# Optimization experiments

Measured on AMD Instinct MI355X. Metric: run time of the kernel, lower is better.

Reference implementation:

```python
import jax, jax.numpy as jnp
import numpy as np


def setup_inputs() -> dict:
    key = jax.random.key(0)
    ks = jax.random.split(key, 7)
    B, T, IN_F = 16384, 64, 48
    F = 32          # feature_size = len(INTERACTIVE_LIST)
    H = 128         # embedding_hidden_size
    TF, TH = T * F, T * H
    scale1 = 1.0 / np.sqrt(TF)
    scale2 = 1.0 / np.sqrt(TH)
    return {
        "x": jax.random.normal(ks[0], (B, T, IN_F), dtype=jnp.float32),
        "W1": jax.random.normal(ks[1], (TF, TH), dtype=jnp.float32) * scale1,
        "b1": jax.random.normal(ks[2], (TH,), dtype=jnp.float32) * scale1,
        "W2": jax.random.normal(ks[3], (TH, TF), dtype=jnp.float32) * scale2,
        "b2": jax.random.normal(ks[4], (TF,), dtype=jnp.float32) * scale2,
        "weight": jax.random.normal(ks[5], (T, F), dtype=jnp.float32),
        "bias": jax.random.normal(ks[6], (F,), dtype=jnp.float32) * (1.0 / np.sqrt(T)),
        "sample_index": jnp.arange(F, dtype=jnp.int32),
    }


def reference(x, W1, b1, W2, b2, weight, bias, sample_index):
    # x: [B, T, IN_F]; gather interactive feature columns -> [B, T, F]
    B = x.shape[0]
    T, F = weight.shape
    xs = jnp.take(x, sample_index, axis=2)            # [B, T, F]
    # pass_linear=True path: MLP on flattened time*feature vector
    h = jax.nn.relu(xs.reshape(B, T * F) @ W1 + b1)   # [B, T*H]; dropout = identity (eval)
    out = (h @ W2 + b2).reshape(B, T, F)              # [B, T, F]
    # vectorized form of the per-sample loop: sum over time of elementwise mul
    emb = jnp.einsum("btf,tf->bf", out, weight) + bias  # [B, F]
    return emb
```

## Files before the change

kernel.cpp:

```cpp
#include <hip/hip_runtime.h>
#include <hip/hip_bf16.h>

#define BATCH 16384
#define TT    64
#define INF   48
#define FF    32
#define TFD   2048
#define THD   8192

typedef __attribute__((ext_vector_type(8))) short bf16x8;
typedef __attribute__((ext_vector_type(4))) short bf16x4;
typedef __attribute__((ext_vector_type(4))) short short4v;
typedef __attribute__((ext_vector_type(4))) float f32x4;

__device__ inline void gload_lds16(const void* g, void* l) {
  __builtin_amdgcn_global_load_lds((const __attribute__((address_space(1))) void*)g,
                                   (__attribute__((address_space(3))) void*)l, 16, 0, 0);
}

__device__ inline f32x4 mfma16x16x16_bf16(bf16x4 a, bf16x4 b, f32x4 c) {
#if __has_builtin(__builtin_amdgcn_mfma_f32_16x16x16bf16_1k)
  return __builtin_amdgcn_mfma_f32_16x16x16bf16_1k(a, b, c, 0, 0, 0);
#else
  asm("v_mfma_f32_16x16x16_bf16 %0, %1, %2, %0" : "+v"(c) : "v"(a), "v"(b));
  return c;
#endif
}

__device__ inline short f32_to_bf16_bits(float x) {
  __hip_bfloat16 h = __float2bfloat16(x);
  return *reinterpret_cast<short*>(&h);
}


__global__ void gather_cast_frag(const float* __restrict__ x, const int* __restrict__ sidx,
                                 __hip_bfloat16* __restrict__ xsf) {
  __shared__ int sx[FF];
  if (threadIdx.x < FF) sx[threadIdx.x] = sidx[threadIdx.x];
  __syncthreads();
  const int b64 = blockIdx.x >> 2;
  const int tq  = blockIdx.x & 3;
  for (int it = 0; it < 16; ++it) {
    const int slot = (tq * 16 + it) * 256 + threadIdx.x;
    const int t  = slot >> 8;
    const int bi = (slot >> 6) & 3;
    const int l  = slot & 63;
    const int lo = l & 15, hi = l >> 4;
    const int row = b64 * 64 + bi * 16 + lo;
    const float* rp = x + ((size_t)row * TT + t) * INF;
    bf16x8 v;
    #pragma unroll
    for (int j = 0; j < 8; ++j) v[j] = f32_to_bf16_bits(rp[sx[hi * 8 + j]]);
    *(bf16x8*)(xsf + ((size_t)b64 * 16384 + slot) * 8) = v;
  }
}

__global__ void transpose_w1(const float* __restrict__ W1, __hip_bfloat16* __restrict__ W1t) {
  __shared__ float tile[64][65];
  const int k0 = blockIdx.x * 64;
  const int n0 = blockIdx.y * 64;
  const int tx = threadIdx.x & 63, ty = threadIdx.x >> 6;
  for (int r = ty; r < 64; r += 4)
    tile[r][tx] = W1[(size_t)(k0 + r) * THD + n0 + tx];
  __syncthreads();
  const int rn = threadIdx.x >> 4;
  const int kq = (threadIdx.x & 15) * 4;
  for (int rr = rn; rr < 64; rr += 16) {
    short4v v;
    #pragma unroll
    for (int i = 0; i < 4; ++i) v[i] = f32_to_bf16_bits(tile[kq + i][rr]);
    *(short4v*)(W1t + (size_t)(n0 + rr) * TFD + k0 + kq) = v;
  }
}

__global__ void make_w2eff(const float* __restrict__ W2, const float* __restrict__ b2,
                           const float* __restrict__ weight, const float* __restrict__ bias,
                           __hip_bfloat16* __restrict__ w2t, float* __restrict__ beff) {
  const int n = blockIdx.x * 8 + (threadIdx.x >> 5);
  const int f = threadIdx.x & 31;
  const float* wr = W2 + (size_t)n * TFD;
  float s = 0.f;
  #pragma unroll 8
  for (int t = 0; t < TT; ++t) s += wr[t * FF + f] * weight[t * FF + f];
  w2t[(size_t)f * THD + n] = __float2bfloat16(s);
  if (blockIdx.x == 0 && threadIdx.x < FF) {
    float sb = bias[f];
    for (int t = 0; t < TT; ++t) sb += b2[t * FF + f] * weight[t * FF + f];
    beff[f] = sb;
  }
}


__device__ inline void stage_w(char* buf, const __hip_bfloat16* __restrict__ w1t,
                               int n0, int k0, int wid, int l) {
  const int sub = l >> 3;
  const int c   = (l & 7) ^ sub;
  const int h   = c >> 2, kc = c & 3;
  const int r0  = wid * 8 + sub;
  const __hip_bfloat16* gw0 = w1t + (size_t)(n0 + 2 * r0 + h) * TFD + k0 + kc * 8;
  const __hip_bfloat16* gw1 = w1t + (size_t)(n0 + 128 + 2 * r0 + h) * TFD + k0 + kc * 8;
  char* lx = buf + wid * 1024;
  gload_lds16(gw0, lx);
  gload_lds16(gw1, lx + 8192);
}

__device__ __forceinline__ void k_iter(char* lds, int t, int n0,
    const char* __restrict__ xbase, const __hip_bfloat16* __restrict__ w1t,
    f32x4 (&acc)[8][4], bf16x8 (&xfu)[4],
    int wbase, int wid, int l, bool do_bar) {
  if (t <= 60) stage_w(lds + ((t + 3) & 7) * 16384, w1t, n0, (t + 3) * 32, wid, l);
  __builtin_amdgcn_sched_barrier(0);
  const char* buf = lds + (t & 7) * 16384;
  bf16x8 w0  = *(const bf16x8*)(buf + wbase);
  bf16x8 w1f = *(const bf16x8*)(buf + wbase + 1024);
  #pragma unroll
  for (int g = 0; g < 4; ++g) {
    bf16x8 nw0, nw1;
    if (g < 3) {
      nw0 = *(const bf16x8*)(buf + wbase + (2 * g + 2) * 1024);
      nw1 = *(const bf16x8*)(buf + wbase + (2 * g + 3) * 1024);
    }
    __builtin_amdgcn_s_setprio(1);
    #pragma unroll
    for (int bi = 0; bi < 4; ++bi)
      acc[2 * g][bi] = __builtin_amdgcn_mfma_f32_16x16x32_bf16(w0, xfu[bi], acc[2 * g][bi], 0, 0, 0);
    #pragma unroll
    for (int bi = 0; bi < 4; ++bi)
      acc[2 * g + 1][bi] = __builtin_amdgcn_mfma_f32_16x16x32_bf16(w1f, xfu[bi], acc[2 * g + 1][bi], 0, 0, 0);
    __builtin_amdgcn_s_setprio(0);
    if (g < 3) { w0 = nw0; w1f = nw1; }
  }
  if (t <= 61) {
    #pragma unroll
    for (int bi = 0; bi < 4; ++bi)
      xfu[bi] = *(const bf16x8*)(xbase + ((t + 2) * 4 + bi) * 1024);
  }
  __builtin_amdgcn_sched_barrier(0);
  if (t <= 60)      asm volatile("s_waitcnt vmcnt(6)" ::: "memory");
  else if (t == 61) asm volatile("s_waitcnt vmcnt(4)" ::: "memory");
  else              asm volatile("s_waitcnt vmcnt(0)" ::: "memory");
  __builtin_amdgcn_sched_barrier(0);
  if (do_bar) {
    __builtin_amdgcn_s_barrier();
    __builtin_amdgcn_sched_barrier(0);
  }
}

__global__ __launch_bounds__(512, 2) void gemm_fused(
    const __hip_bfloat16* __restrict__ xsf,
    const __hip_bfloat16* __restrict__ w1t,
    const float* __restrict__ b1,
    const __hip_bfloat16* __restrict__ w2t,
    float* __restrict__ partial)
{
  __shared__ __align__(16) char lds[131072];
  const int tid = threadIdx.x;
  const int wid = tid >> 6, l = tid & 63;
  const int mq = wid >> 2, bq = wid & 3;
  const int lo = l & 15, hi = l >> 4;
  const int rl = lo >> 1;
  const int cofs = (((((lo & 1) << 2) | hi) ^ rl) << 4);
  const int strip = blockIdx.x & 7;
  const int bt = blockIdx.x >> 3;
  const int b0 = bt * 256;

  const int wbase = ((mq << 6) + rl) * 128 + cofs;
  const char* xbase = (const char*)xsf + ((size_t)(bt * 4 + bq) * 16384 + l) * 16;

  f32x4 acc2[2][4];
  #pragma unroll
  for (int fi = 0; fi < 2; ++fi)
    #pragma unroll
    for (int bi = 0; bi < 4; ++bi) { f32x4 z = {0.f,0.f,0.f,0.f}; acc2[fi][bi] = z; }

  for (int s = 0; s < 4; ++s) {
    const int n0 = strip * 1024 + s * 256;

    f32x4 acc[8][4];
    #pragma unroll
    for (int mi = 0; mi < 8; ++mi)
      #pragma unroll
      for (int bi = 0; bi < 4; ++bi) { f32x4 z = {0.f,0.f,0.f,0.f}; acc[mi][bi] = z; }

    bf16x8 xfA[4], xfB[4];
    stage_w(lds, w1t, n0, 0, wid, l);
    __builtin_amdgcn_sched_barrier(0);
    #pragma unroll
    for (int bi = 0; bi < 4; ++bi) xfA[bi] = *(const bf16x8*)(xbase + (0 * 4 + bi) * 1024);
    __builtin_amdgcn_sched_barrier(0);
    stage_w(lds + 16384, w1t, n0, 32, wid, l);
    __builtin_amdgcn_sched_barrier(0);
    #pragma unroll
    for (int bi = 0; bi < 4; ++bi) xfB[bi] = *(const bf16x8*)(xbase + (1 * 4 + bi) * 1024);
    __builtin_amdgcn_sched_barrier(0);
    stage_w(lds + 32768, w1t, n0, 64, wid, l);
    __builtin_amdgcn_sched_barrier(0);
    asm volatile("s_waitcnt vmcnt(8)" ::: "memory");
    __builtin_amdgcn_sched_barrier(0);
    __builtin_amdgcn_s_barrier();
    __builtin_amdgcn_sched_barrier(0);

    for (int tt = 0; tt < 64; tt += 2) {
      k_iter(lds, tt,     n0, xbase, w1t, acc, xfA, wbase, wid, l, false);
      k_iter(lds, tt + 1, n0, xbase, w1t, acc, xfB, wbase, wid, l, true);
    }

    #pragma unroll
    for (int mi = 0; mi < 8; ++mi) {
      const int nbase = n0 + (mq << 7) + (mi << 4);
      const float4 b1v = *(const float4*)(b1 + nbase + (hi << 2));
      bf16x4 p[4];
      #pragma unroll
      for (int bi = 0; bi < 4; ++bi) {
        bf16x4 pk;
        #pragma unroll
        for (int j = 0; j < 4; ++j) {
          float v = acc[mi][bi][j] + ((const float*)&b1v)[j];
          v = v > 0.f ? v : 0.f;
          pk[j] = f32_to_bf16_bits(v);
        }
        p[bi] = pk;
      }
      bf16x4 a2[2];
      #pragma unroll
      for (int fi = 0; fi < 2; ++fi)
        a2[fi] = *(const bf16x4*)(w2t + (size_t)(fi * 16 + lo) * THD + nbase + (hi << 2));
      #pragma unroll
      for (int fi = 0; fi < 2; ++fi)
        #pragma unroll
        for (int bi = 0; bi < 4; ++bi)
          acc2[fi][bi] = mfma16x16x16_bf16(a2[fi], p[bi], acc2[fi][bi]);
    }
  }

  float* sm = (float*)lds;
  if (mq == 1) {
    #pragma unroll
    for (int fi = 0; fi < 2; ++fi)
      #pragma unroll
      for (int bi = 0; bi < 4; ++bi)
        *(f32x4*)(sm + ((bq << 6) + (bi << 4) + lo) * 32 + fi * 16 + (hi << 2)) = acc2[fi][bi];
  }
  __syncthreads();
  if (mq == 0) {
    #pragma unroll
    for (int fi = 0; fi < 2; ++fi)
      #pragma unroll
      for (int bi = 0; bi < 4; ++bi) {
        f32x4 other = *(const f32x4*)(sm + ((bq << 6) + (bi << 4) + lo) * 32 + fi * 16 + (hi << 2));
        f32x4 v = acc2[fi][bi] + other;
        *(f32x4*)(partial + ((size_t)strip * BATCH + b0 + (bq << 6) + (bi << 4) + lo) * FF + fi * 16 + (hi << 2)) = v;
      }
  }
}

__global__ void reduce_partial(const float* __restrict__ partial, const float* __restrict__ beff,
                               float* __restrict__ out) {
  const int idx = blockIdx.x * 256 + threadIdx.x;
  float s = beff[idx & 31];
  #pragma unroll
  for (int c = 0; c < 8; ++c) s += partial[(size_t)c * BATCH * FF + idx];
  out[idx] = s;
}


extern "C" void kernel_launch(void* const* d_in, const int* in_sizes, int n_in,
                              void* d_out, int out_size, void* d_ws, size_t ws_size,
                              hipStream_t stream) {
  const float* x      = (const float*)d_in[0];
  const float* W1     = (const float*)d_in[1];
  const float* b1     = (const float*)d_in[2];
  const float* W2     = (const float*)d_in[3];
  const float* b2     = (const float*)d_in[4];
  const float* weight = (const float*)d_in[5];
  const float* bias   = (const float*)d_in[6];
  const int*   sidx   = (const int*)d_in[7];

  char* ws = (char*)d_ws;
  __hip_bfloat16* xsf  = (__hip_bfloat16*)ws;
  __hip_bfloat16* w1t  = (__hip_bfloat16*)(ws + 67108864);
  __hip_bfloat16* w2t  = (__hip_bfloat16*)(ws + 100663296);
  float*          beff = (float*)(ws + 101187584);
  float*          part = (float*)(ws + 101188608);

  hipLaunchKernelGGL(gather_cast_frag, dim3(1024), dim3(256), 0, stream, x, sidx, xsf);
  hipLaunchKernelGGL(transpose_w1, dim3(32, 128), dim3(256), 0, stream, W1, w1t);
  hipLaunchKernelGGL(make_w2eff,   dim3(1024),    dim3(256), 0, stream, W2, b2, weight, bias, w2t, beff);
  hipLaunchKernelGGL(gemm_fused,   dim3(512),     dim3(512), 0, stream, xsf, w1t, b1, w2t, part);
  hipLaunchKernelGGL(reduce_partial, dim3(2048),  dim3(256), 0, stream, part, beff, (float*)d_out);
}
```

Baseline: 614.2 us.

## Restage W1 pipeline into 64-wide K chunks with staggered half order per wave group

Restructures the first GEMM's K loop so each stage loads 64 K-values into a 32KB LDS slot, using a 4-slot ring instead of 8 single 32-wide slots. Wave groups (mq) process the two halves of each chunk in opposite order, which spreads LDS bank and x-load traffic across time. Barriers drop to one every two stages. The aim is fewer barriers and better overlap of global-to-LDS loads with MFMA work. The cost is more intricate vmcnt accounting, which risks hazards if the waitcnt values are wrong.

```diff
diff --git a/kernel.cpp b/kernel.cpp
--- a/kernel.cpp
+++ b/kernel.cpp
@@ -12,6 +12,9 @@
 typedef __attribute__((ext_vector_type(4))) short bf16x4;
 typedef __attribute__((ext_vector_type(4))) short short4v;
 typedef __attribute__((ext_vector_type(4))) float f32x4;
+
+#define SCHED __builtin_amdgcn_sched_barrier(0)
+#define VMW(n) asm volatile("s_waitcnt vmcnt(" #n ")" ::: "memory")
 
 __device__ inline void gload_lds16(const void* g, void* l) {
   __builtin_amdgcn_global_load_lds((const __attribute__((address_space(1))) void*)g,
@@ -104,21 +107,28 @@
   gload_lds16(gw1, lx + 8192);
 }
 
-__device__ __forceinline__ void k_iter(char* lds, int t, int n0,
-    const char* __restrict__ xbase, const __hip_bfloat16* __restrict__ w1t,
-    f32x4 (&acc)[8][4], bf16x8 (&xfu)[4],
-    int wbase, int wid, int l, bool do_bar) {
-  if (t <= 60) stage_w(lds + ((t + 3) & 7) * 16384, w1t, n0, (t + 3) * 32, wid, l);
-  __builtin_amdgcn_sched_barrier(0);
-  const char* buf = lds + (t & 7) * 16384;
-  bf16x8 w0  = *(const bf16x8*)(buf + wbase);
-  bf16x8 w1f = *(const bf16x8*)(buf + wbase + 1024);
+__device__ inline void stage_w64(char* buf, const __hip_bfloat16* __restrict__ w1t,
+                                 int n0, int k0, int wid, int l) {
+  stage_w(buf,         w1t, n0, k0,      wid, l);
+  stage_w(buf + 16384, w1t, n0, k0 + 32, wid, l);
+}
+
+__device__ __forceinline__ void refill(bf16x8 (&xf)[4], const char* __restrict__ xbase, int u) {
+  #pragma unroll
+  for (int bi = 0; bi < 4; ++bi)
+    xf[bi] = *(const bf16x8*)(xbase + (u * 4 + bi) * 1024);
+}
+
+__device__ __forceinline__ void half_mfma(const char* hbuf, f32x4 (&acc)[8][4],
+                                          bf16x8 (&xfu)[4], int wbase) {
+  bf16x8 w0  = *(const bf16x8*)(hbuf + wbase);
+  bf16x8 w1f = *(const bf16x8*)(hbuf + wbase + 1024);
   #pragma unroll
   for (int g = 0; g < 4; ++g) {
     bf16x8 nw0, nw1;
     if (g < 3) {
-      nw0 = *(const bf16x8*)(buf + wbase + (2 * g + 2) * 1024);
-      nw1 = *(const bf16x8*)(buf + wbase + (2 * g + 3) * 1024);
+      nw0 = *(const bf16x8*)(hbuf + wbase + (2 * g + 2) * 1024);
+      nw1 = *(const bf16x8*)(hbuf + wbase + (2 * g + 3) * 1024);
     }
     __builtin_amdgcn_s_setprio(1);
     #pragma unroll
@@ -129,20 +139,6 @@
       acc[2 * g + 1][bi] = __builtin_amdgcn_mfma_f32_16x16x32_bf16(w1f, xfu[bi], acc[2 * g + 1][bi], 0, 0, 0);
     __builtin_amdgcn_s_setprio(0);
     if (g < 3) { w0 = nw0; w1f = nw1; }
-  }
-  if (t <= 61) {
-    #pragma unroll
-    for (int bi = 0; bi < 4; ++bi)
-      xfu[bi] = *(const bf16x8*)(xbase + ((t + 2) * 4 + bi) * 1024);
-  }
-  __builtin_amdgcn_sched_barrier(0);
-  if (t <= 60)      asm volatile("s_waitcnt vmcnt(6)" ::: "memory");
-  else if (t == 61) asm volatile("s_waitcnt vmcnt(4)" ::: "memory");
-  else              asm volatile("s_waitcnt vmcnt(0)" ::: "memory");
-  __builtin_amdgcn_sched_barrier(0);
-  if (do_bar) {
-    __builtin_amdgcn_s_barrier();
-    __builtin_amdgcn_sched_barrier(0);
   }
 }
 
@@ -182,27 +178,62 @@
       #pragma unroll
       for (int bi = 0; bi < 4; ++bi) { f32x4 z = {0.f,0.f,0.f,0.f}; acc[mi][bi] = z; }
 
-    bf16x8 xfA[4], xfB[4];
-    stage_w(lds, w1t, n0, 0, wid, l);
-    __builtin_amdgcn_sched_barrier(0);
-    #pragma unroll
-    for (int bi = 0; bi < 4; ++bi) xfA[bi] = *(const bf16x8*)(xbase + (0 * 4 + bi) * 1024);
-    __builtin_amdgcn_sched_barrier(0);
-    stage_w(lds + 16384, w1t, n0, 32, wid, l);
-    __builtin_amdgcn_sched_barrier(0);
-    #pragma unroll
-    for (int bi = 0; bi < 4; ++bi) xfB[bi] = *(const bf16x8*)(xbase + (1 * 4 + bi) * 1024);
-    __builtin_amdgcn_sched_barrier(0);
-    stage_w(lds + 32768, w1t, n0, 64, wid, l);
-    __builtin_amdgcn_sched_barrier(0);
-    asm volatile("s_waitcnt vmcnt(8)" ::: "memory");
-    __builtin_amdgcn_sched_barrier(0);
-    __builtin_amdgcn_s_barrier();
-    __builtin_amdgcn_sched_barrier(0);
-
-    for (int tt = 0; tt < 64; tt += 2) {
-      k_iter(lds, tt,     n0, xbase, w1t, acc, xfA, wbase, wid, l, false);
-      k_iter(lds, tt + 1, n0, xbase, w1t, acc, xfB, wbase, wid, l, true);
+    bf16x8 xf0[4], xf1[4];
+    stage_w64(lds,         w1t, n0, 0,  wid, l); SCHED;
+    stage_w64(lds + 32768, w1t, n0, 64, wid, l); SCHED;
+    if (mq == 0) { refill(xf0, xbase, 0); SCHED; refill(xf1, xbase, 1); }
+    else         { refill(xf1, xbase, 1); SCHED; refill(xf0, xbase, 0); }
+    SCHED;
+    VMW(12); SCHED;
+    __builtin_amdgcn_s_barrier(); SCHED;
+
+    for (int t = 0; t < 30; ++t) {
+      stage_w64(lds + ((t + 2) & 3) * 32768, w1t, n0, (t + 2) * 64, wid, l);
+      SCHED;
+      const char* buf = lds + (t & 3) * 32768;
+      if (mq == 0) {
+        VMW(8); SCHED;
+        half_mfma(buf, acc, xf0, wbase);
+        refill(xf0, xbase, 2 * t + 2); SCHED;
+        VMW(8); SCHED;
+        half_mfma(buf + 16384, acc, xf1, wbase);
+        refill(xf1, xbase, 2 * t + 3); SCHED;
+        VMW(8); SCHED;
+      } else {
+        VMW(8); SCHED;
+        half_mfma(buf + 16384, acc, xf1, wbase);
+        refill(xf1, xbase, 2 * t + 3); SCHED;
+        VMW(8); SCHED;
+        half_mfma(buf, acc, xf0, wbase);
+        refill(xf0, xbase, 2 * t + 2); SCHED;
+        VMW(8); SCHED;
+      }
+      if (!(t & 1)) { __builtin_amdgcn_s_barrier(); SCHED; }
+    }
+    {
+      const char* buf = lds + 2 * 32768;
+      if (mq == 0) {
+        VMW(4); SCHED; half_mfma(buf, acc, xf0, wbase);
+        refill(xf0, xbase, 62); SCHED;
+        VMW(4); SCHED; half_mfma(buf + 16384, acc, xf1, wbase);
+        refill(xf1, xbase, 63); SCHED;
+      } else {
+        VMW(4); SCHED; half_mfma(buf + 16384, acc, xf1, wbase);
+        refill(xf1, xbase, 63); SCHED;
+        VMW(4); SCHED; half_mfma(buf, acc, xf0, wbase);
+        refill(xf0, xbase, 62); SCHED;
+      }
+      __builtin_amdgcn_s_barrier(); SCHED;
+    }
+    {
+      const char* buf = lds + 3 * 32768;
+      if (mq == 0) {
+        VMW(4); SCHED; half_mfma(buf, acc, xf0, wbase);
+        SCHED; VMW(0); SCHED; half_mfma(buf + 16384, acc, xf1, wbase);
+      } else {
+        VMW(4); SCHED; half_mfma(buf + 16384, acc, xf1, wbase);
+        SCHED; VMW(0); SCHED; half_mfma(buf, acc, xf0, wbase);
+      }
     }
 
     #pragma unroll
```

Result: slower. 898.6 us (+46.3%).

## Stage x tiles through LDS and restructure K loop into two barrier-synced phases

Applied to the files above, without the earlier changes.

Activation tiles are now copied into LDS with direct global-to-LDS loads shared across the block, instead of each wave loading its own x fragments into registers from global memory. The K loop becomes a 4-buffer LDS ring with two compute phases per step, each opened by a block barrier, with the W and x staging interleaved between them in a ping-pong style schedule. This cuts redundant global x traffic and register pressure. The cost is several more block barriers per iteration and a shallower W prefetch distance (2 ahead instead of 3).

```diff
diff --git a/kernel.cpp b/kernel.cpp
--- a/kernel.cpp
+++ b/kernel.cpp
@@ -12,6 +12,10 @@
 typedef __attribute__((ext_vector_type(4))) short bf16x4;
 typedef __attribute__((ext_vector_type(4))) short short4v;
 typedef __attribute__((ext_vector_type(4))) float f32x4;
+
+#define SCHED __builtin_amdgcn_sched_barrier(0)
+#define VMW(n) asm volatile("s_waitcnt vmcnt(" #n ")" ::: "memory")
+#define LGKM0  asm volatile("s_waitcnt lgkmcnt(0)" ::: "memory")
 
 __device__ inline void gload_lds16(const void* g, void* l) {
   __builtin_amdgcn_global_load_lds((const __attribute__((address_space(1))) void*)g,
@@ -104,46 +108,12 @@
   gload_lds16(gw1, lx + 8192);
 }
 
-__device__ __forceinline__ void k_iter(char* lds, int t, int n0,
-    const char* __restrict__ xbase, const __hip_bfloat16* __restrict__ w1t,
-    f32x4 (&acc)[8][4], bf16x8 (&xfu)[4],
-    int wbase, int wid, int l, bool do_bar) {
-  if (t <= 60) stage_w(lds + ((t + 3) & 7) * 16384, w1t, n0, (t + 3) * 32, wid, l);
-  __builtin_amdgcn_sched_barrier(0);
-  const char* buf = lds + (t & 7) * 16384;
-  bf16x8 w0  = *(const bf16x8*)(buf + wbase);
-  bf16x8 w1f = *(const bf16x8*)(buf + wbase + 1024);
-  #pragma unroll
-  for (int g = 0; g < 4; ++g) {
-    bf16x8 nw0, nw1;
-    if (g < 3) {
-      nw0 = *(const bf16x8*)(buf + wbase + (2 * g + 2) * 1024);
-      nw1 = *(const bf16x8*)(buf + wbase + (2 * g + 3) * 1024);
-    }
-    __builtin_amdgcn_s_setprio(1);
-    #pragma unroll
-    for (int bi = 0; bi < 4; ++bi)
-      acc[2 * g][bi] = __builtin_amdgcn_mfma_f32_16x16x32_bf16(w0, xfu[bi], acc[2 * g][bi], 0, 0, 0);
-    #pragma unroll
-    for (int bi = 0; bi < 4; ++bi)
-      acc[2 * g + 1][bi] = __builtin_amdgcn_mfma_f32_16x16x32_bf16(w1f, xfu[bi], acc[2 * g + 1][bi], 0, 0, 0);
-    __builtin_amdgcn_s_setprio(0);
-    if (g < 3) { w0 = nw0; w1f = nw1; }
-  }
-  if (t <= 61) {
-    #pragma unroll
-    for (int bi = 0; bi < 4; ++bi)
-      xfu[bi] = *(const bf16x8*)(xbase + ((t + 2) * 4 + bi) * 1024);
-  }
-  __builtin_amdgcn_sched_barrier(0);
-  if (t <= 60)      asm volatile("s_waitcnt vmcnt(6)" ::: "memory");
-  else if (t == 61) asm volatile("s_waitcnt vmcnt(4)" ::: "memory");
-  else              asm volatile("s_waitcnt vmcnt(0)" ::: "memory");
-  __builtin_amdgcn_sched_barrier(0);
-  if (do_bar) {
-    __builtin_amdgcn_s_barrier();
-    __builtin_amdgcn_sched_barrier(0);
-  }
+__device__ inline void stage_x(char* bufX, const char* __restrict__ xg, int t, int wid, int l) {
+  const int g = wid >> 1, bi0 = (wid & 1) * 2;
+  const char* src = xg + (size_t)g * 262144 + ((t * 4 + bi0) * 1024) + l * 16;
+  char* dst = bufX + g * 4096 + bi0 * 1024;
+  gload_lds16(src, dst);
+  gload_lds16(src + 1024, dst + 1024);
 }
 
 __global__ __launch_bounds__(512, 2) void gemm_fused(
@@ -165,7 +135,8 @@
   const int b0 = bt * 256;
 
   const int wbase = ((mq << 6) + rl) * 128 + cofs;
-  const char* xbase = (const char*)xsf + ((size_t)(bt * 4 + bq) * 16384 + l) * 16;
+  const int xoff  = (bq << 12) + l * 16;
+  const char* xg  = (const char*)xsf + (size_t)(bt * 4) * 262144;
 
   f32x4 acc2[2][4];
   #pragma unroll
@@ -182,27 +153,84 @@
       #pragma unroll
       for (int bi = 0; bi < 4; ++bi) { f32x4 z = {0.f,0.f,0.f,0.f}; acc[mi][bi] = z; }
 
-    bf16x8 xfA[4], xfB[4];
     stage_w(lds, w1t, n0, 0, wid, l);
-    __builtin_amdgcn_sched_barrier(0);
-    #pragma unroll
-    for (int bi = 0; bi < 4; ++bi) xfA[bi] = *(const bf16x8*)(xbase + (0 * 4 + bi) * 1024);
-    __builtin_amdgcn_sched_barrier(0);
-    stage_w(lds + 16384, w1t, n0, 32, wid, l);
-    __builtin_amdgcn_sched_barrier(0);
-    #pragma unroll
-    for (int bi = 0; bi < 4; ++bi) xfB[bi] = *(const bf16x8*)(xbase + (1 * 4 + bi) * 1024);
-    __builtin_amdgcn_sched_barrier(0);
-    stage_w(lds + 32768, w1t, n0, 64, wid, l);
-    __builtin_amdgcn_sched_barrier(0);
-    asm volatile("s_waitcnt vmcnt(8)" ::: "memory");
-    __builtin_amdgcn_sched_barrier(0);
-    __builtin_amdgcn_s_barrier();
-    __builtin_amdgcn_sched_barrier(0);
-
-    for (int tt = 0; tt < 64; tt += 2) {
-      k_iter(lds, tt,     n0, xbase, w1t, acc, xfA, wbase, wid, l, false);
-      k_iter(lds, tt + 1, n0, xbase, w1t, acc, xfB, wbase, wid, l, true);
+    stage_x(lds + 16384, xg, 0, wid, l);
+    SCHED;
+    stage_w(lds + 32768, w1t, n0, 32, wid, l);
+    stage_x(lds + 32768 + 16384, xg, 1, wid, l);
+    SCHED;
+    VMW(4); SCHED;
+    __builtin_amdgcn_s_barrier(); SCHED;
+
+    for (int t = 0; t < 64; ++t) {
+      char* buf  = lds + (size_t)(t & 3) * 32768;
+      char* nbuf = lds + (size_t)((t + 2) & 3) * 32768;
+
+      bf16x8 wf0 = *(const bf16x8*)(buf + wbase);
+      bf16x8 wf1 = *(const bf16x8*)(buf + wbase + 1024);
+      bf16x8 wf2 = *(const bf16x8*)(buf + wbase + 2048);
+      bf16x8 wf3 = *(const bf16x8*)(buf + wbase + 3072);
+      bf16x8 xf0 = *(const bf16x8*)(buf + 16384 + xoff);
+      bf16x8 xf1 = *(const bf16x8*)(buf + 16384 + xoff + 1024);
+      bf16x8 xf2 = *(const bf16x8*)(buf + 16384 + xoff + 2048);
+      bf16x8 xf3 = *(const bf16x8*)(buf + 16384 + xoff + 3072);
+      if (t < 62) stage_w(nbuf, w1t, n0, (t + 2) * 32, wid, l);
+      SCHED;
+      __builtin_amdgcn_s_barrier();
+      LGKM0; SCHED;
+      __builtin_amdgcn_s_setprio(1);
+      acc[0][0] = __builtin_amdgcn_mfma_f32_16x16x32_bf16(wf0, xf0, acc[0][0], 0, 0, 0);
+      acc[0][1] = __builtin_amdgcn_mfma_f32_16x16x32_bf16(wf0, xf1, acc[0][1], 0, 0, 0);
+      acc[0][2] = __builtin_amdgcn_mfma_f32_16x16x32_bf16(wf0, xf2, acc[0][2], 0, 0, 0);
+      acc[0][3] = __builtin_amdgcn_mfma_f32_16x16x32_bf16(wf0, xf3, acc[0][3], 0, 0, 0);
+      acc[1][0] = __builtin_amdgcn_mfma_f32_16x16x32_bf16(wf1, xf0, acc[1][0], 0, 0, 0);
+      acc[1][1] = __builtin_amdgcn_mfma_f32_16x16x32_bf16(wf1, xf1, acc[1][1], 0, 0, 0);
+      acc[1][2] = __builtin_amdgcn_mfma_f32_16x16x32_bf16(wf1, xf2, acc[1][2], 0, 0, 0);
+      acc[1][3] = __builtin_amdgcn_mfma_f32_16x16x32_bf16(wf1, xf3, acc[1][3], 0, 0, 0);
+      acc[2][0] = __builtin_amdgcn_mfma_f32_16x16x32_bf16(wf2, xf0, acc[2][0], 0, 0, 0);
+      acc[2][1] = __builtin_amdgcn_mfma_f32_16x16x32_bf16(wf2, xf1, acc[2][1], 0, 0, 0);
+      acc[2][2] = __builtin_amdgcn_mfma_f32_16x16x32_bf16(wf2, xf2, acc[2][2], 0, 0, 0);
+      acc[2][3] = __builtin_amdgcn_mfma_f32_16x16x32_bf16(wf2, xf3, acc[2][3], 0, 0, 0);
+      acc[3][0] = __builtin_amdgcn_mfma_f32_16x16x32_bf16(wf3, xf0, acc[3][0], 0, 0, 0);
+      acc[3][1] = __builtin_amdgcn_mfma_f32_16x16x32_bf16(wf3, xf1, acc[3][1], 0, 0, 0);
+      acc[3][2] = __builtin_amdgcn_mfma_f32_16x16x32_bf16(wf3, xf2, acc[3][2], 0, 0, 0);
+      acc[3][3] = __builtin_amdgcn_mfma_f32_16x16x32_bf16(wf3, xf3, acc[3][3], 0, 0, 0);
+      __builtin_amdgcn_s_setprio(0);
+      SCHED;
+      __builtin_amdgcn_s_barrier();
+
+      bf16x8 wf4 = *(const bf16x8*)(buf + wbase + 4096);
+      bf16x8 wf5 = *(const bf16x8*)(buf + wbase + 5120);
+      bf16x8 wf6 = *(const bf16x8*)(buf + wbase + 6144);
+      bf16x8 wf7 = *(const bf16x8*)(buf + wbase + 7168);
+      if (t < 62) stage_x(nbuf + 16384, xg, t + 2, wid, l);
+      SCHED;
+      __builtin_amdgcn_s_barrier();
+      LGKM0; SCHED;
+      __builtin_amdgcn_s_setprio(1);
+      acc[4][0] = __builtin_amdgcn_mfma_f32_16x16x32_bf16(wf4, xf0, acc[4][0], 0, 0, 0);
+      acc[4][1] = __builtin_amdgcn_mfma_f32_16x16x32_bf16(wf4, xf1, acc[4][1], 0, 0, 0);
+      acc[4][2] = __builtin_amdgcn_mfma_f32_16x16x32_bf16(wf4, xf2, acc[4][2], 0, 0, 0);
+      acc[4][3] = __builtin_amdgcn_mfma_f32_16x16x32_bf16(wf4, xf3, acc[4][3], 0, 0, 0);
+      acc[5][0] = __builtin_amdgcn_mfma_f32_16x16x32_bf16(wf5, xf0, acc[5][0], 0, 0, 0);
+      acc[5][1] = __builtin_amdgcn_mfma_f32_16x16x32_bf16(wf5, xf1, acc[5][1], 0, 0, 0);
+      acc[5][2] = __builtin_amdgcn_mfma_f32_16x16x32_bf16(wf5, xf2, acc[5][2], 0, 0, 0);
+      acc[5][3] = __builtin_amdgcn_mfma_f32_16x16x32_bf16(wf5, xf3, acc[5][3], 0, 0, 0);
+      acc[6][0] = __builtin_amdgcn_mfma_f32_16x16x32_bf16(wf6, xf0, acc[6][0], 0, 0, 0);
+      acc[6][1] = __builtin_amdgcn_mfma_f32_16x16x32_bf16(wf6, xf1, acc[6][1], 0, 0, 0);
+      acc[6][2] = __builtin_amdgcn_mfma_f32_16x16x32_bf16(wf6, xf2, acc[6][2], 0, 0, 0);
+      acc[6][3] = __builtin_amdgcn_mfma_f32_16x16x32_bf16(wf6, xf3, acc[6][3], 0, 0, 0);
+      acc[7][0] = __builtin_amdgcn_mfma_f32_16x16x32_bf16(wf7, xf0, acc[7][0], 0, 0, 0);
+      acc[7][1] = __builtin_amdgcn_mfma_f32_16x16x32_bf16(wf7, xf1, acc[7][1], 0, 0, 0);
+      acc[7][2] = __builtin_amdgcn_mfma_f32_16x16x32_bf16(wf7, xf2, acc[7][2], 0, 0, 0);
+      acc[7][3] = __builtin_amdgcn_mfma_f32_16x16x32_bf16(wf7, xf3, acc[7][3], 0, 0, 0);
+      __builtin_amdgcn_s_setprio(0);
+      SCHED;
+      if (t < 62)       { VMW(4); }
+      else if (t == 62) { VMW(0); }
+      SCHED;
+      __builtin_amdgcn_s_barrier();
+      SCHED;
     }
 
     #pragma unroll
```

New measurement: 621.3 us. About the same (+1.1%).

## Flatten N-strip loop into one continuous W1 staging pipeline across strips

Applied to the files above, without the earlier changes.

Merges the four per-strip K loops into one 256-iteration pipeline, so W1 tile prefetch for the next strip starts while the current strip finishes. This removes the pipeline drain and refill (prologue stalls and barriers) at each strip boundary. The bias/ReLU/second-GEMM epilogue now runs inside the loop every 64 iterations while later prefetches are in flight. A __syncthreads is added before LDS reuse for the final reduction. The risks are added register pressure and the epilogue's global loads interfering with the vmcnt waits.

```diff
diff --git a/kernel.cpp b/kernel.cpp
--- a/kernel.cpp
+++ b/kernel.cpp
@@ -12,6 +12,9 @@
 typedef __attribute__((ext_vector_type(4))) short bf16x4;
 typedef __attribute__((ext_vector_type(4))) short short4v;
 typedef __attribute__((ext_vector_type(4))) float f32x4;
+
+#define SCHED __builtin_amdgcn_sched_barrier(0)
+#define VMW(n) asm volatile("s_waitcnt vmcnt(" #n ")" ::: "memory")
 
 __device__ inline void gload_lds16(const void* g, void* l) {
   __builtin_amdgcn_global_load_lds((const __attribute__((address_space(1))) void*)g,
@@ -104,13 +107,17 @@
   gload_lds16(gw1, lx + 8192);
 }
 
-__device__ __forceinline__ void k_iter(char* lds, int t, int n0,
+__device__ __forceinline__ void k_iter(char* lds, int v, int strip,
     const char* __restrict__ xbase, const __hip_bfloat16* __restrict__ w1t,
     f32x4 (&acc)[8][4], bf16x8 (&xfu)[4],
     int wbase, int wid, int l, bool do_bar) {
-  if (t <= 60) stage_w(lds + ((t + 3) & 7) * 16384, w1t, n0, (t + 3) * 32, wid, l);
-  __builtin_amdgcn_sched_barrier(0);
-  const char* buf = lds + (t & 7) * 16384;
+  if (v <= 252) {
+    const int vs = v + 3;
+    stage_w(lds + (size_t)(vs & 7) * 16384, w1t,
+            strip * 1024 + (vs >> 6) * 256, (vs & 63) * 32, wid, l);
+  }
+  SCHED;
+  const char* buf = lds + (size_t)(v & 7) * 16384;
   bf16x8 w0  = *(const bf16x8*)(buf + wbase);
   bf16x8 w1f = *(const bf16x8*)(buf + wbase + 1024);
   #pragma unroll
@@ -130,19 +137,19 @@
     __builtin_amdgcn_s_setprio(0);
     if (g < 3) { w0 = nw0; w1f = nw1; }
   }
-  if (t <= 61) {
+  if (v <= 253) {
+    const int u = (v + 2) & 63;
     #pragma unroll
     for (int bi = 0; bi < 4; ++bi)
-      xfu[bi] = *(const bf16x8*)(xbase + ((t + 2) * 4 + bi) * 1024);
-  }
-  __builtin_amdgcn_sched_barrier(0);
-  if (t <= 60)      asm volatile("s_waitcnt vmcnt(6)" ::: "memory");
-  else if (t == 61) asm volatile("s_waitcnt vmcnt(4)" ::: "memory");
-  else              asm volatile("s_waitcnt vmcnt(0)" ::: "memory");
-  __builtin_amdgcn_sched_barrier(0);
+      xfu[bi] = *(const bf16x8*)(xbase + (u * 4 + bi) * 1024);
+  }
+  SCHED;
+  if (v <= 252)      { VMW(6); }
+  else if (v == 253) { VMW(4); }
+  else               { VMW(0); }
+  SCHED;
   if (do_bar) {
-    __builtin_amdgcn_s_barrier();
-    __builtin_amdgcn_sched_barrier(0);
+    __builtin_amdgcn_s_barrier(); SCHED;
   }
 }
 
@@ -173,67 +180,67 @@
     #pragma unroll
     for (int bi = 0; bi < 4; ++bi) { f32x4 z = {0.f,0.f,0.f,0.f}; acc2[fi][bi] = z; }
 
-  for (int s = 0; s < 4; ++s) {
-    const int n0 = strip * 1024 + s * 256;
-
-    f32x4 acc[8][4];
-    #pragma unroll
-    for (int mi = 0; mi < 8; ++mi)
+  f32x4 acc[8][4];
+  #pragma unroll
+  for (int mi = 0; mi < 8; ++mi)
+    #pragma unroll
+    for (int bi = 0; bi < 4; ++bi) { f32x4 z = {0.f,0.f,0.f,0.f}; acc[mi][bi] = z; }
+
+  bf16x8 xfA[4], xfB[4];
+  stage_w(lds, w1t, strip * 1024, 0, wid, l);
+  SCHED;
+  #pragma unroll
+  for (int bi = 0; bi < 4; ++bi) xfA[bi] = *(const bf16x8*)(xbase + (0 * 4 + bi) * 1024);
+  SCHED;
+  stage_w(lds + 16384, w1t, strip * 1024, 32, wid, l);
+  SCHED;
+  #pragma unroll
+  for (int bi = 0; bi < 4; ++bi) xfB[bi] = *(const bf16x8*)(xbase + (1 * 4 + bi) * 1024);
+  SCHED;
+  stage_w(lds + 32768, w1t, strip * 1024, 64, wid, l);
+  SCHED;
+  VMW(8); SCHED;
+  __builtin_amdgcn_s_barrier(); SCHED;
+
+  for (int vv = 0; vv < 256; vv += 2) {
+    k_iter(lds, vv,     strip, xbase, w1t, acc, xfA, wbase, wid, l, false);
+    k_iter(lds, vv + 1, strip, xbase, w1t, acc, xfB, wbase, wid, l, true);
+
+    if ((vv & 63) == 62) {
+      const int n0e = strip * 1024 + (vv >> 6) * 256;
       #pragma unroll
-      for (int bi = 0; bi < 4; ++bi) { f32x4 z = {0.f,0.f,0.f,0.f}; acc[mi][bi] = z; }
-
-    bf16x8 xfA[4], xfB[4];
-    stage_w(lds, w1t, n0, 0, wid, l);
-    __builtin_amdgcn_sched_barrier(0);
-    #pragma unroll
-    for (int bi = 0; bi < 4; ++bi) xfA[bi] = *(const bf16x8*)(xbase + (0 * 4 + bi) * 1024);
-    __builtin_amdgcn_sched_barrier(0);
-    stage_w(lds + 16384, w1t, n0, 32, wid, l);
-    __builtin_amdgcn_sched_barrier(0);
-    #pragma unroll
-    for (int bi = 0; bi < 4; ++bi) xfB[bi] = *(const bf16x8*)(xbase + (1 * 4 + bi) * 1024);
-    __builtin_amdgcn_sched_barrier(0);
-    stage_w(lds + 32768, w1t, n0, 64, wid, l);
-    __builtin_amdgcn_sched_barrier(0);
-    asm volatile("s_waitcnt vmcnt(8)" ::: "memory");
-    __builtin_amdgcn_sched_barrier(0);
-    __builtin_amdgcn_s_barrier();
-    __builtin_amdgcn_sched_barrier(0);
-
-    for (int tt = 0; tt < 64; tt += 2) {
-      k_iter(lds, tt,     n0, xbase, w1t, acc, xfA, wbase, wid, l, false);
-      k_iter(lds, tt + 1, n0, xbase, w1t, acc, xfB, wbase, wid, l, true);
+      for (int mi = 0; mi < 8; ++mi) {
+        const int nbase = n0e + (mq << 7) + (mi << 4);
+        const float4 b1v = *(const float4*)(b1 + nbase + (hi << 2));
+        bf16x4 p[4];
+        #pragma unroll
+        for (int bi = 0; bi < 4; ++bi) {
+          bf16x4 pk;
+          #pragma unroll
+          for (int j = 0; j < 4; ++j) {
+            float v = acc[mi][bi][j] + ((const float*)&b1v)[j];
+            v = v > 0.f ? v : 0.f;
+            pk[j] = f32_to_bf16_bits(v);
+          }
+          p[bi] = pk;
+        }
+        bf16x4 a2[2];
+        #pragma unroll
+        for (int fi = 0; fi < 2; ++fi)
+          a2[fi] = *(const bf16x4*)(w2t + (size_t)(fi * 16 + lo) * THD + nbase + (hi << 2));
+        #pragma unroll
+        for (int fi = 0; fi < 2; ++fi)
+          #pragma unroll
+          for (int bi = 0; bi < 4; ++bi)
+            acc2[fi][bi] = mfma16x16x16_bf16(a2[fi], p[bi], acc2[fi][bi]);
+        #pragma unroll
+        for (int bi = 0; bi < 4; ++bi) { f32x4 z = {0.f,0.f,0.f,0.f}; acc[mi][bi] = z; }
+      }
     }
-
-    #pragma unroll
-    for (int mi = 0; mi < 8; ++mi) {
-      const int nbase = n0 + (mq << 7) + (mi << 4);
-      const float4 b1v = *(const float4*)(b1 + nbase + (hi << 2));
-      bf16x4 p[4];
-      #pragma unroll
-      for (int bi = 0; bi < 4; ++bi) {
-        bf16x4 pk;
-        #pragma unroll
-        for (int j = 0; j < 4; ++j) {
-          float v = acc[mi][bi][j] + ((const float*)&b1v)[j];
-          v = v > 0.f ? v : 0.f;
-          pk[j] = f32_to_bf16_bits(v);
-        }
-        p[bi] = pk;
-      }
-      bf16x4 a2[2];
-      #pragma unroll
-      for (int fi = 0; fi < 2; ++fi)
-        a2[fi] = *(const bf16x4*)(w2t + (size_t)(fi * 16 + lo) * THD + nbase + (hi << 2));
-      #pragma unroll
-      for (int fi = 0; fi < 2; ++fi)
-        #pragma unroll
-        for (int bi = 0; bi < 4; ++bi)
-          acc2[fi][bi] = mfma16x16x16_bf16(a2[fi], p[bi], acc2[fi][bi]);
-    }
   }
 
   float* sm = (float*)lds;
+  __syncthreads();
   if (mq == 1) {
     #pragma unroll
     for (int fi = 0; fi < 2; ++fi)
```

After: 597.4 us, median of 3. 2.7% less time.
